# Kernel optimization log

Hardware: AMD Instinct MI355X
Metric: run time of the kernel (lower is better)

## Reference

```python
import jax, jax.numpy as jnp
import numpy as np

NUM_HEADS = 12
LN_EPS = 1e-5
SM_EPS = 1e-6


def layer_norm(x, w, b):
    m = x.mean(-1, keepdims=True)
    v = ((x - m) ** 2).mean(-1, keepdims=True)
    return (x - m) / jnp.sqrt(v + LN_EPS) * w + b


def softmax_with_policy(attn, policy):
    # attn: [B,H,N,N], policy: [B,N,1]
    B, H, N, _ = attn.shape
    attn_policy = policy.reshape(B, 1, 1, N)
    eye = jnp.eye(N, dtype=attn.dtype)[None, None]
    attn_policy = attn_policy + (1.0 - attn_policy) * eye
    m = attn.max(axis=-1, keepdims=True)
    e = jnp.exp(attn - m) * attn_policy
    return (e + SM_EPS / N) / (e.sum(axis=-1, keepdims=True) + SM_EPS)


def create_ys(ncdf, n_ref):
    # ncdf: [B, N-1]; returns ys: [B, n_ref-1]
    B = ncdf.shape[0]
    ys = jnp.linspace(0.0, 1.0, n_ref - 1, dtype=ncdf.dtype)[None, :]
    ys_start = jnp.min(ncdf + (ncdf == 0).astype(ncdf.dtype) * 1e8, axis=1, keepdims=True)
    steps = jnp.arange(n_ref - 1, dtype=ncdf.dtype)[None, :]
    return ys_start + (ys * (n_ref - 2) - ys_start * steps) / (n_ref - 2)


def get_unique_indices(indices, max_value):
    # duplicate indices are replaced by max_value, then re-sorted
    B = indices.shape[0]
    s = jnp.sort(indices, axis=1)
    shifted = jnp.concatenate([s[:, 1:], jnp.ones((B, 1), s.dtype)], axis=1)
    uniq = jnp.where(shifted == s, max_value, s)
    return jnp.sort(uniq, axis=1)


def ats_block(x, policy, norm1_w, norm1_b, qkv_w, proj_w, proj_b,
              norm2_w, norm2_b, fc1_w, fc1_b, fc2_w, fc2_b,
              n_tokens, n_ref_tokens):
    B, N, C = x.shape
    H = NUM_HEADS
    dh = C // H
    scale = dh ** -0.5

    xn = layer_norm(x, norm1_w, norm1_b)
    qkv = (xn @ qkv_w).reshape(B, N, 3, H, dh).transpose(2, 0, 3, 1, 4)  # [3,B,H,N,dh]
    qkv = qkv * policy[None, :, None, :, :]
    q, k, v = qkv[0], qkv[1], qkv[2]

    attn = softmax_with_policy(jnp.einsum('bhnd,bhmd->bhnm', q, k) * scale, policy)

    # --- score assignment ---
    v_norm = jnp.linalg.norm(v.transpose(0, 2, 1, 3).reshape(B, N, C), axis=2)  # [B,N]
    sig = attn[:, :, 0, :].sum(axis=1) * v_norm      # CLS attention row summed over heads
    sig = sig[:, 1:]
    sig = sig / sig.sum(axis=1, keepdims=True)
    order = jnp.argsort(sig, axis=1)                 # ascending
    sorted_scores = jnp.take_along_axis(sig, order, axis=1)

    # --- inverse transform sampling ---
    cdf = jnp.cumsum(sorted_scores, axis=1)
    cmin = cdf.min(axis=1, keepdims=True)
    cmax = cdf.max(axis=1, keepdims=True)
    ncdf = (cdf - cmin) / (cmax - cmin)              # [B, N-1]
    ys = create_ys(ncdf, n_ref_tokens)               # [B, n_ref-1]
    diff = (n_ref_tokens - 1) - (N - 1)
    ncdf_p = jnp.pad(ncdf, ((0, 0), (diff, 0))) if diff > 0 else ncdf
    tokens_to_pick = jnp.argmin(jnp.abs(ys[:, :, None] - ncdf_p[:, None, :]), axis=2) - diff

    uniq = get_unique_indices(tokens_to_pick, N - 1)[:, :N - 1]
    ui = uniq[:, :n_tokens - 1]                      # [B, n_tokens-1]

    # reorder attn rows / raw tokens by significance order, pad a zero row at N-1
    oidx = jnp.broadcast_to(order[:, None, :, None], (B, H, N - 1, N))
    attn_sorted = jnp.take_along_axis(attn[:, :, 1:, :], oidx, axis=2)
    attn_tmp = jnp.pad(attn_sorted, ((0, 0), (0, 0), (0, 1), (0, 0)))
    rx_sorted = jnp.take_along_axis(x[:, 1:, :], jnp.broadcast_to(order[:, :, None], (B, N - 1, C)), axis=1)
    rx_tmp = jnp.pad(rx_sorted, ((0, 0), (0, 1), (0, 0)))

    uidx = jnp.broadcast_to(ui[:, None, :, None], (B, H, n_tokens - 1, N))
    attn_sel = jnp.take_along_axis(attn_tmp, uidx, axis=2)
    rx_sel = jnp.take_along_axis(rx_tmp, jnp.broadcast_to(ui[:, :, None], (B, n_tokens - 1, C)), axis=1)

    attn_new = jnp.concatenate([attn[:, :, 0:1, :], attn_sel], axis=2)     # [B,H,n_tokens,N]
    selected_x = jnp.concatenate([x[:, 0:1, :], rx_sel], axis=1)           # [B,n_tokens,C]
    pol_new = (ui != N - 1).astype(x.dtype)[:, :, None]
    pol_new = jnp.pad(pol_new, ((0, 0), (1, 0), (0, 0)), constant_values=1.0)  # [B,n_tokens,1]

    out = jnp.einsum('bhnm,bhmd->bhnd', attn_new, v)
    out = out.transpose(0, 2, 1, 3).reshape(B, n_tokens, C)
    out = (out @ proj_w + proj_b) * pol_new

    x2 = selected_x + out
    h = jax.nn.gelu(layer_norm(x2, norm2_w, norm2_b) @ fc1_w + fc1_b, approximate=False)
    x2 = x2 + (h @ fc2_w + fc2_b) * pol_new
    return x2, pol_new


def setup_inputs() -> dict:
    key = jax.random.key(0)
    ks = jax.random.split(key, 6)
    B, N, C = 8, 785, 768
    init = lambda k, sh, fan: jax.random.normal(k, sh, jnp.float32) * (fan ** -0.5)
    return {
        'x': jax.random.normal(ks[0], (B, N, C), jnp.float32),
        'policy': jnp.ones((B, N, 1), jnp.float32),
        'norm1_w': jnp.ones((C,), jnp.float32),
        'norm1_b': jnp.zeros((C,), jnp.float32),
        'qkv_w': init(ks[1], (C, 3 * C), C),
        'proj_w': init(ks[2], (C, C), C),
        'proj_b': jnp.zeros((C,), jnp.float32),
        'norm2_w': jnp.ones((C,), jnp.float32),
        'norm2_b': jnp.zeros((C,), jnp.float32),
        'fc1_w': init(ks[3], (C, 4 * C), C),
        'fc1_b': jnp.zeros((4 * C,), jnp.float32),
        'fc2_w': init(ks[4], (4 * C, C), 4 * C),
        'fc2_b': jnp.zeros((C,), jnp.float32),
        'n_tokens': 393,
        'n_ref_tokens': 785,
    }


def reference(x, policy, norm1_w, norm1_b, qkv_w, proj_w, proj_b,
              norm2_w, norm2_b, fc1_w, fc1_b, fc2_w, fc2_b,
              n_tokens, n_ref_tokens):
    return ats_block(x, policy, norm1_w, norm1_b, qkv_w, proj_w, proj_b,
                     norm2_w, norm2_b, fc1_w, fc1_b, fc2_w, fc2_b,
                     int(n_tokens), int(n_ref_tokens))
```

## Files before the change

kernel.cpp:

```cpp
#include <hip/hip_runtime.h>
#include <hip/hip_bf16.h>
#include <float.h>
#include <math.h>
#include <stdint.h>

constexpr int B_   = 8;
constexpr int N_   = 785;
constexpr int C_   = 768;
constexpr int H_   = 12;
constexpr int DH_  = 64;
constexpr int NT_  = 393;
constexpr int QKVC = 3 * C_;
constexpr int BN   = B_ * N_;
constexpr int BT   = B_ * NT_;
constexpr int MSEL = N_ - 1;
constexpr float  SCALE_F = 0.125f;
constexpr double LNEPS   = 1e-5;
constexpr double SMEPS   = 1e-6;

#define DEV static __device__ __forceinline__

typedef __hip_bfloat16 bf16;
typedef __attribute__((ext_vector_type(8))) short frag8;
typedef __attribute__((ext_vector_type(4))) float facc4;

DEV short f2b(float v) { return (short)__hip_bfloat16_raw(__float2bfloat16(v)).x; }
DEV float b2f(short s) {
  union { unsigned int u; float f; } cv;
  cv.u = ((unsigned int)(unsigned short)s) << 16;
  return cv.f;
}
DEV float gelu_exact(float v) { return 0.5f * v * (1.0f + erff(v * 0.70710678118654752f)); }

DEV double blockReduceSumD(double v, double* scratch, int nw) {
#pragma unroll
  for (int o = 32; o; o >>= 1) v += __shfl_xor(v, o);
  int lane = threadIdx.x & 63, wid = threadIdx.x >> 6;
  __syncthreads();
  if (lane == 0) scratch[wid] = v;
  __syncthreads();
  double r = scratch[0];
  for (int i = 1; i < nw; i++) r += scratch[i];
  return r;
}
DEV double blockReduceMaxD(double v, double* scratch, int nw) {
#pragma unroll
  for (int o = 32; o; o >>= 1) v = fmax(v, __shfl_xor(v, o));
  int lane = threadIdx.x & 63, wid = threadIdx.x >> 6;
  __syncthreads();
  if (lane == 0) scratch[wid] = v;
  __syncthreads();
  double r = scratch[0];
  for (int i = 1; i < nw; i++) r = fmax(r, scratch[i]);
  return r;
}
DEV float blockReduceSumF(float v, float* scratch, int nw) {
#pragma unroll
  for (int o = 32; o; o >>= 1) v += __shfl_xor(v, o);
  int lane = threadIdx.x & 63, wid = threadIdx.x >> 6;
  __syncthreads();
  if (lane == 0) scratch[wid] = v;
  __syncthreads();
  float r = scratch[0];
  for (int i = 1; i < nw; i++) r += scratch[i];
  return r;
}
DEV float blockReduceMaxF(float v, float* scratch, int nw) {
#pragma unroll
  for (int o = 32; o; o >>= 1) v = fmaxf(v, __shfl_xor(v, o));
  int lane = threadIdx.x & 63, wid = threadIdx.x >> 6;
  __syncthreads();
  if (lane == 0) scratch[wid] = v;
  __syncthreads();
  float r = scratch[0];
  for (int i = 1; i < nw; i++) r = fmaxf(r, scratch[i]);
  return r;
}

__global__ __launch_bounds__(256) void ln1_kernel(
    const float* __restrict__ x, const float* __restrict__ w, const float* __restrict__ b,
    double* __restrict__ xn64, bf16* __restrict__ xnb) {
  int row = blockIdx.x;
  int t = threadIdx.x;
  __shared__ double scr[8];
  const float* xr = x + (size_t)row * C_;
  double vals[3];
#pragma unroll
  for (int i = 0; i < 3; i++) vals[i] = (double)xr[t + i * 256];
  double s = vals[0] + vals[1] + vals[2];
  s = blockReduceSumD(s, scr, 4);
  double mean = s / (double)C_;
  double vs = 0.0;
#pragma unroll
  for (int i = 0; i < 3; i++) { double d = vals[i] - mean; vs += d * d; }
  vs = blockReduceSumD(vs, scr, 4);
  double inv = 1.0 / sqrt(vs / (double)C_ + LNEPS);
#pragma unroll
  for (int i = 0; i < 3; i++) {
    int c = t + i * 256;
    double o = (vals[i] - mean) * inv * (double)w[c] + (double)b[c];
    xn64[(size_t)row * C_ + c] = o;
    xnb[(size_t)row * C_ + c] = __float2bfloat16((float)o);
  }
}

__global__ __launch_bounds__(256) void transpose_bf16(
    const float* __restrict__ W, bf16* __restrict__ Wt, int K, int N) {
  __shared__ float tile[32][33];
  int k0 = blockIdx.y * 32, n0 = blockIdx.x * 32;
  int tx = threadIdx.x & 31, ty = threadIdx.x >> 5;
  for (int i = ty; i < 32; i += 8) {
    int k = k0 + i, n = n0 + tx;
    tile[i][tx] = (k < K && n < N) ? W[(size_t)k * N + n] : 0.f;
  }
  __syncthreads();
  for (int i = ty; i < 32; i += 8) {
    int n = n0 + i, k = k0 + tx;
    if (n < N && k < K) Wt[(size_t)n * K + k] = __float2bfloat16(tile[tx][i]);
  }
}

__global__ __launch_bounds__(256) void gemm_bf16(
    const bf16* __restrict__ A, const bf16* __restrict__ Bt,
    float* __restrict__ Cc, const float* __restrict__ bias,
    const float* __restrict__ rowscale, int M, int K, int Ncols,
    int mode, const float* __restrict__ xg, const int* __restrict__ selidx_,
    const float* __restrict__ poln_, const float* __restrict__ res) {
  __shared__ short As[64][40];
  __shared__ short Bs[64][40];
  const short* Ap = (const short*)A;
  const short* Bp = (const short*)Bt;
  int t = threadIdx.x;
  int n0 = blockIdx.x * 64;
  int m0 = blockIdx.y * 64;
  int w = t >> 6, l = t & 63;
  int srow = t >> 2;
  int koff = (t & 3) * 8;
  facc4 acc[4] = {{0, 0, 0, 0}, {0, 0, 0, 0}, {0, 0, 0, 0}, {0, 0, 0, 0}};
  int frow = (l & 15);
  int fk = (l >> 4) * 8;
  for (int k0 = 0; k0 < K; k0 += 32) {
    {
      int4 av = make_int4(0, 0, 0, 0);
      if (m0 + srow < M)
        av = *(const int4*)(Ap + (size_t)(m0 + srow) * K + k0 + koff);
      *(int4*)(&As[srow][koff]) = av;
      int4 bv = *(const int4*)(Bp + (size_t)(n0 + srow) * K + k0 + koff);
      *(int4*)(&Bs[srow][koff]) = bv;
    }
    __syncthreads();
    frag8 a = *(frag8*)(&As[w * 16 + frow][fk]);
#pragma unroll
    for (int nt = 0; nt < 4; nt++) {
      frag8 bfr = *(frag8*)(&Bs[nt * 16 + frow][fk]);
      acc[nt] = __builtin_amdgcn_mfma_f32_16x16x32_bf16(a, bfr, acc[nt], 0, 0, 0);
    }
    __syncthreads();
  }
#pragma unroll
  for (int reg = 0; reg < 4; reg++) {
    int row = m0 + w * 16 + (l >> 4) * 4 + reg;
    if (row >= M) continue;
    float rs = (mode == 0 && rowscale) ? rowscale[row] : 1.f;
    float pn = (mode != 0) ? poln_[row] : 0.f;
    int rsel = (mode == 1) ? selidx_[row] : 0;
    int bI = (mode == 1) ? (row / NT_) : 0;
#pragma unroll
    for (int nt = 0; nt < 4; nt++) {
      int col = n0 + nt * 16 + (l & 15);
      float v = acc[nt][reg];
      if (bias) v += bias[col];
      float outv;
      if (mode == 0) {
        outv = v * rs;
      } else if (mode == 1) {
        float sx = (rsel >= 0) ? xg[(size_t)(bI * N_ + rsel) * C_ + col] : 0.f;
        outv = sx + v * pn;
      } else {
        outv = res[(size_t)row * Ncols + col] + v * pn;
      }
      Cc[(size_t)row * Ncols + col] = outv;
    }
  }
}

__global__ __launch_bounds__(256) void gemm128(
    const bf16* __restrict__ A, const bf16* __restrict__ Bt,
    float* __restrict__ Cc, const float* __restrict__ bias,
    const float* __restrict__ rowscale, int M, int K, int Ncols,
    bf16* __restrict__ gelu_bf) {
  __shared__ short As[128][40];
  __shared__ short Bs[128][40];
  const short* Ap = (const short*)A;
  const short* Bp = (const short*)Bt;
  int t = threadIdx.x;
  int n0 = blockIdx.x * 128;
  int m0 = blockIdx.y * 128;
  int w = t >> 6, l = t & 63;
  int wr = w >> 1, wc = w & 1;
  int srow = t >> 1;
  int koff = (t & 1) * 16;
  int fr = l & 15, fk = (l >> 4) * 8;
  facc4 acc[4][4] = {};
  for (int k0 = 0; k0 < K; k0 += 32) {
    int4 av0 = make_int4(0, 0, 0, 0), av1 = make_int4(0, 0, 0, 0);
    if (m0 + srow < M) {
      const short* ap = Ap + (size_t)(m0 + srow) * K + k0 + koff;
      av0 = *(const int4*)ap;
      av1 = *(const int4*)(ap + 8);
    }
    const short* bp = Bp + (size_t)(n0 + srow) * K + k0 + koff;
    int4 bv0 = *(const int4*)bp;
    int4 bv1 = *(const int4*)(bp + 8);
    *(int4*)(&As[srow][koff])     = av0;
    *(int4*)(&As[srow][koff + 8]) = av1;
    *(int4*)(&Bs[srow][koff])     = bv0;
    *(int4*)(&Bs[srow][koff + 8]) = bv1;
    __syncthreads();
    frag8 af[4], bf[4];
#pragma unroll
    for (int i = 0; i < 4; i++) af[i] = *(frag8*)(&As[wr * 64 + i * 16 + fr][fk]);
#pragma unroll
    for (int j = 0; j < 4; j++) bf[j] = *(frag8*)(&Bs[wc * 64 + j * 16 + fr][fk]);
#pragma unroll
    for (int i = 0; i < 4; i++)
#pragma unroll
      for (int j = 0; j < 4; j++)
        acc[i][j] = __builtin_amdgcn_mfma_f32_16x16x32_bf16(af[i], bf[j], acc[i][j], 0, 0, 0);
    __syncthreads();
  }
#pragma unroll
  for (int i = 0; i < 4; i++) {
#pragma unroll
    for (int reg = 0; reg < 4; reg++) {
      int row = m0 + wr * 64 + i * 16 + (l >> 4) * 4 + reg;
      if (row >= M) continue;
      float rs = rowscale ? rowscale[row] : 1.f;
#pragma unroll
      for (int j = 0; j < 4; j++) {
        int col = n0 + wc * 64 + j * 16 + fr;
        float v = acc[i][j][reg];
        if (bias) v += bias[col];
        if (gelu_bf) {
          gelu_bf[(size_t)row * Ncols + col] = __float2bfloat16(gelu_exact(v));
        } else {
          v *= rs;
          Cc[(size_t)row * Ncols + col] = v;
        }
      }
    }
  }
}

__global__ __launch_bounds__(256) void q0_kernel(
    const double* __restrict__ xn64, const float* __restrict__ qkvw,
    const float* __restrict__ policy, double* __restrict__ q064) {
  int b = blockIdx.x;
  int jc = blockIdx.y;
  int t = threadIdx.x;
  int jl = t & 63, ks = t >> 6;
  __shared__ double x0[C_];
  __shared__ double part[4][64];
  for (int i = t; i < C_; i += 256) x0[i] = xn64[(size_t)(b * N_) * C_ + i];
  __syncthreads();
  int j = jc * 64 + jl;
  const float* wp = qkvw + j;
  double a = 0.0;
  int c0 = ks * 192;
#pragma unroll 8
  for (int c = c0; c < c0 + 192; c++) a += x0[c] * (double)wp[(size_t)c * QKVC];
  part[ks][jl] = a;
  __syncthreads();
  if (t < 64) {
    double pol = (double)policy[b * N_];
    q064[b * C_ + jc * 64 + t] =
        (part[0][t] + part[1][t] + part[2][t] + part[3][t]) * pol;
  }
}

__global__ __launch_bounds__(256) void g_kernel(
    const double* __restrict__ q064, const float* __restrict__ qkvw,
    double* __restrict__ g64) {
  int bh = blockIdx.x;
  int b = bh / H_, h = bh % H_;
  int t = threadIdx.x;
  __shared__ double qh[DH_];
  if (t < DH_) qh[t] = q064[b * C_ + h * DH_ + t];
  __syncthreads();
  for (int c = t; c < C_; c += 256) {
    const float* wp = qkvw + (size_t)c * QKVC + C_ + h * DH_;
    double a = 0.0;
#pragma unroll 8
    for (int d = 0; d < DH_; d++) a += qh[d] * (double)wp[d];
    g64[(size_t)bh * C_ + c] = a;
  }
}

__global__ __launch_bounds__(256) void logits_kernel(
    const double* __restrict__ xn64, const double* __restrict__ g64,
    const float* __restrict__ policy, double* __restrict__ l64) {
  int row = blockIdx.x;
  int b = row / N_;
  int n = row % N_;
  int t = threadIdx.x;
  int w = t >> 6, lane = t & 63;
  __shared__ double xr[C_];
  for (int i = t; i < C_; i += 256) xr[i] = xn64[(size_t)row * C_ + i];
  __syncthreads();
  double pol = (double)policy[row];
#pragma unroll
  for (int hh = 0; hh < 3; hh++) {
    int h = w + hh * 4;
    const double* gp = g64 + (size_t)(b * H_ + h) * C_;
    double p = 0.0;
#pragma unroll 4
    for (int i = lane; i < C_; i += 64) p += xr[i] * gp[i];
#pragma unroll
    for (int o = 32; o; o >>= 1) p += __shfl_xor(p, o);
    if (lane == 0) l64[(size_t)(b * H_ + h) * N_ + n] = 0.125 * pol * p;
  }
}

__global__ __launch_bounds__(256) void vnorm_kernel(
    const double* __restrict__ xn64, const float* __restrict__ qkvw,
    const float* __restrict__ policy, double* __restrict__ vnorm2) {
  __shared__ double scr[8];
  int r0 = blockIdx.x * 8;
  int t = threadIdx.x;
  double acc[8][3] = {};
  const double* xb = xn64 + (size_t)r0 * C_;
  for (int c = 0; c < C_; c += 2) {
    const float* wp0 = qkvw + (size_t)c * QKVC + 2 * C_;
    const float* wp1 = wp0 + QKVC;
    double w00 = (double)wp0[t], w01 = (double)wp0[t + 256], w02 = (double)wp0[t + 512];
    double w10 = (double)wp1[t], w11 = (double)wp1[t + 256], w12 = (double)wp1[t + 512];
#pragma unroll
    for (int r = 0; r < 8; r++) {
      double x0 = xb[(size_t)r * C_ + c];
      double x1 = xb[(size_t)r * C_ + c + 1];
      acc[r][0] += x0 * w00; acc[r][1] += x0 * w01; acc[r][2] += x0 * w02;
      acc[r][0] += x1 * w10; acc[r][1] += x1 * w11; acc[r][2] += x1 * w12;
    }
  }
#pragma unroll
  for (int r = 0; r < 8; r++) {
    double p = acc[r][0] * acc[r][0] + acc[r][1] * acc[r][1] + acc[r][2] * acc[r][2];
    double s = blockReduceSumD(p, scr, 4);
    if (t == 0) {
      double pol = (double)policy[r0 + r];
      vnorm2[r0 + r] = s * pol * pol;
    }
  }
}

__global__ __launch_bounds__(256) void softmax0_kernel(
    double* __restrict__ l64, const float* __restrict__ policy) {
  int bh = blockIdx.x;
  int b = bh / H_;
  double* lp = l64 + (size_t)bh * N_;
  __shared__ double scr[8];
  int t = threadIdx.x;
  double mx = -1e300;
  for (int n = t; n < N_; n += 256) mx = fmax(mx, lp[n]);
  mx = blockReduceMaxD(mx, scr, 4);
  double ssum = 0.0;
  for (int n = t; n < N_; n += 256) {
    double pol = (double)policy[b * N_ + n];
    double w = (n == 0) ? 1.0 : pol;
    double e = exp(lp[n] - mx) * w;
    lp[n] = e;
    ssum += e;
  }
  ssum = blockReduceSumD(ssum, scr, 4);
  double denom = ssum + SMEPS;
  double addc = SMEPS / (double)N_;
  for (int n = t; n < N_; n += 256) lp[n] = (lp[n] + addc) / denom;
}

__global__ __launch_bounds__(1024) void select_kernel(
    const double* __restrict__ p0, const double* __restrict__ vnorm2,
    int* __restrict__ selidx, float* __restrict__ poln, float* __restrict__ out_pol) {
  int b = blockIdx.x;
  int t = threadIdx.x;
  __shared__ double sigv[MSEL];
  __shared__ double svals[MSEL];
  __shared__ double nc[MSEL];
  __shared__ int    ord[MSEL];
  __shared__ int    pick[MSEL];
  __shared__ int    spick[MSEL];
  __shared__ int    uq[MSEL];
  __shared__ int    suq[MSEL];
  __shared__ double sh_ys;

  if (t < MSEL) {
    int n = t + 1;
    double s = 0.0;
#pragma unroll
    for (int h = 0; h < H_; h++) s += p0[(size_t)(b * H_ + h) * N_ + n];
    sigv[t] = s * sqrt(vnorm2[b * N_ + n]);
  }
  __syncthreads();
  if (t < MSEL) {
    double v = sigv[t];
    int rank = 0;
    for (int i = 0; i < MSEL; i++) {
      double vi = sigv[i];
      rank += (vi < v) || (vi == v && i < t);
    }
    ord[rank] = t;
    svals[rank] = v;
  }
  __syncthreads();
  if (t == 0) {
    double a = 0.0;
    for (int i = 0; i < MSEL; i++) { a += svals[i]; svals[i] = a; }
  }
  __syncthreads();
  {
    double c0 = svals[0], cN = svals[MSEL - 1];
    if (t < MSEL) nc[t] = (svals[t] - c0) / (cN - c0);
  }
  __syncthreads();
  if (t == 0) {
    double m = 1e300;
    for (int i = 0; i < MSEL; i++) {
      double v = nc[i];
      if (v == 0.0) v += 100000000.0;
      m = fmin(m, v);
    }
    sh_ys = m;
  }
  __syncthreads();
  if (t < MSEL) {
    double s = sh_ys;
    double ysj = (t == MSEL - 1) ? 1.0 : (double)t / 783.0;
    double y = s + (ysj * 783.0 - s * (double)t) / 783.0;
    double bd = 1e300;
    int bi = 0;
    for (int i = 0; i < MSEL; i++) {
      double d = fabs(y - nc[i]);
      if (d < bd) { bd = d; bi = i; }
    }
    pick[t] = bi;
  }
  __syncthreads();
  if (t < MSEL) {
    int p = pick[t];
    int rank = 0;
    for (int i = 0; i < MSEL; i++) {
      int pi = pick[i];
      rank += (pi < p) || (pi == p && i < t);
    }
    spick[rank] = p;
  }
  __syncthreads();
  if (t < MSEL) {
    int s = spick[t];
    int nxt = (t < MSEL - 1) ? spick[t + 1] : 1;
    uq[t] = (nxt == s) ? MSEL : s;
  }
  __syncthreads();
  if (t < MSEL) {
    int u = uq[t];
    int rank = 0;
    for (int i = 0; i < MSEL; i++) {
      int ui = uq[i];
      rank += (ui < u) || (ui == u && i < t);
    }
    suq[rank] = u;
  }
  __syncthreads();
  if (t < NT_) {
    int sel, polI;
    if (t == 0) { sel = 0; polI = 1; }
    else {
      int ut = suq[t - 1];
      polI = (ut != MSEL) ? 1 : 0;
      sel = polI ? (ord[ut] + 1) : -1;
    }
    selidx[b * NT_ + t] = sel;
    poln[b * NT_ + t] = (float)polI;
    out_pol[b * NT_ + t] = (float)polI;
  }
}

__global__ __launch_bounds__(256) void flash_kernel(
    const float* __restrict__ qkv, const int* __restrict__ selidx,
    const float* __restrict__ policy, bf16* __restrict__ attn_bf) {
  int bh = blockIdx.y;
  int b = bh / H_, h = bh % H_;
  int j0 = blockIdx.x * 64;
  int t = threadIdx.x;
  int w = t >> 6, l = t & 63;
  __shared__ short Qs[64][72];
  __shared__ short Ks[64][72];
  __shared__ short Ps[64][72];
  __shared__ short Vs[64][72];
  __shared__ float pol_s[64];
  __shared__ float Vsum[64];

  {
    int jr = t >> 2, d0 = (t & 3) * 16;
    int j = j0 + jr;
    int r = (j < NT_) ? selidx[b * NT_ + j] : -1;
    if (r < 0) r = 0;
    const float* qp = qkv + (size_t)(b * N_ + r) * QKVC + h * DH_ + d0;
#pragma unroll
    for (int i = 0; i < 16; i++) Qs[jr][d0 + i] = f2b(qp[i]);
  }
  if (t < 64) Vsum[t] = 0.f;

  int frow = l & 15, fk = (l >> 4) * 8;
  int base_r = w * 16 + (l >> 4) * 4;
  int coln = l & 15;

  int rrow[4];
#pragma unroll
  for (int r = 0; r < 4; r++) {
    int j = j0 + base_r + r;
    rrow[r] = (j < NT_) ? selidx[b * NT_ + j] : -1;
  }
  float m_run[4] = {-1e30f, -1e30f, -1e30f, -1e30f};
  float s_run[4] = {0.f, 0.f, 0.f, 0.f};
  facc4 Oacc[4] = {{0, 0, 0, 0}, {0, 0, 0, 0}, {0, 0, 0, 0}, {0, 0, 0, 0}};

  for (int n0 = 0; n0 < 832; n0 += 64) {
    {
      int nr = t >> 2, d0 = (t & 3) * 16;
      int n = n0 + nr;
      bool ok = n < N_;
      const float* kp = qkv + (size_t)(b * N_ + (ok ? n : 0)) * QKVC + C_ + h * DH_ + d0;
#pragma unroll
      for (int i = 0; i < 16; i++) Ks[nr][d0 + i] = f2b(ok ? kp[i] : 0.f);
    }
    if (t < 64) {
      int n = n0 + t;
      pol_s[t] = (n < N_) ? policy[b * N_ + n] : 0.f;
    }
    __syncthreads();

    facc4 Sacc[4] = {{0, 0, 0, 0}, {0, 0, 0, 0}, {0, 0, 0, 0}, {0, 0, 0, 0}};
#pragma unroll
    for (int k0 = 0; k0 < 64; k0 += 32) {
      frag8 a = *(frag8*)(&Qs[w * 16 + frow][k0 + fk]);
#pragma unroll
      for (int nt = 0; nt < 4; nt++) {
        frag8 bb = *(frag8*)(&Ks[nt * 16 + frow][k0 + fk]);
        Sacc[nt] = __builtin_amdgcn_mfma_f32_16x16x32_bf16(a, bb, Sacc[nt], 0, 0, 0);
      }
    }
    float S[4][4];
    float tmax[4] = {-1e30f, -1e30f, -1e30f, -1e30f};
#pragma unroll
    for (int nt = 0; nt < 4; nt++) {
#pragma unroll
      for (int r = 0; r < 4; r++) {
        int n = n0 + nt * 16 + coln;
        float v = (n < N_) ? Sacc[nt][r] * SCALE_F : -1e30f;
        S[nt][r] = v;
        tmax[r] = fmaxf(tmax[r], v);
      }
    }
#pragma unroll
    for (int o = 1; o < 16; o <<= 1) {
#pragma unroll
      for (int r = 0; r < 4; r++) tmax[r] = fmaxf(tmax[r], __shfl_xor(tmax[r], o));
    }
    float m_new[4], scl[4], psum[4];
#pragma unroll
    for (int r = 0; r < 4; r++) {
      m_new[r] = fmaxf(m_run[r], tmax[r]);
      scl[r] = expf(m_run[r] - m_new[r]);
      psum[r] = 0.f;
    }
#pragma unroll
    for (int nt = 0; nt < 4; nt++) {
      float pol = pol_s[nt * 16 + coln];
      int n = n0 + nt * 16 + coln;
#pragma unroll
      for (int r = 0; r < 4; r++) {
        float wgt = (n == rrow[r]) ? 1.f : pol;
        float e = expf(S[nt][r] - m_new[r]) * wgt;
        S[nt][r] = e;
        psum[r] += e;
      }
    }
#pragma unroll
    for (int o = 1; o < 16; o <<= 1) {
#pragma unroll
      for (int r = 0; r < 4; r++) psum[r] += __shfl_xor(psum[r], o);
    }
#pragma unroll
    for (int r = 0; r < 4; r++) {
      s_run[r] = s_run[r] * scl[r] + psum[r];
      m_run[r] = m_new[r];
    }
    __syncthreads();

#pragma unroll
    for (int nt = 0; nt < 4; nt++) {
#pragma unroll
      for (int r = 0; r < 4; r++) Ps[base_r + r][nt * 16 + coln] = f2b(S[nt][r]);
    }
    {
      int nr = t >> 2, d0 = (t & 3) * 16;
      int n = n0 + nr;
      bool ok = n < N_;
      const float* vp = qkv + (size_t)(b * N_ + (ok ? n : 0)) * QKVC + 2 * C_ + h * DH_ + d0;
#pragma unroll
      for (int i = 0; i < 16; i++) Vs[d0 + i][nr] = f2b(ok ? vp[i] : 0.f);
    }
    __syncthreads();

    if (t < 64) {
      float a = 0.f;
#pragma unroll 16
      for (int k = 0; k < 64; k++) a += b2f(Vs[t][k]);
      Vsum[t] += a;
    }
#pragma unroll
    for (int dt = 0; dt < 4; dt++) {
#pragma unroll
      for (int r = 0; r < 4; r++) Oacc[dt][r] *= scl[r];
    }
#pragma unroll
    for (int k0 = 0; k0 < 64; k0 += 32) {
      frag8 a = *(frag8*)(&Ps[w * 16 + frow][k0 + fk]);
#pragma unroll
      for (int dt = 0; dt < 4; dt++) {
        frag8 bb = *(frag8*)(&Vs[dt * 16 + frow][k0 + fk]);
        Oacc[dt] = __builtin_amdgcn_mfma_f32_16x16x32_bf16(a, bb, Oacc[dt], 0, 0, 0);
      }
    }
  }
  __syncthreads();
  float addc = 1e-6f / (float)N_;
#pragma unroll
  for (int r = 0; r < 4; r++) {
    int j = j0 + base_r + r;
    if (j >= NT_) continue;
    float denom = s_run[r] + 1e-6f;
#pragma unroll
    for (int dt = 0; dt < 4; dt++) {
      int d = dt * 16 + coln;
      float val = (Oacc[dt][r] + addc * Vsum[d]) / denom;
      attn_bf[(size_t)(b * NT_ + j) * C_ + h * DH_ + d] = __float2bfloat16(val);
    }
  }
}

__global__ __launch_bounds__(256) void ln2_kernel(
    const float* __restrict__ xin, const float* __restrict__ w, const float* __restrict__ b,
    bf16* __restrict__ xoutb) {
  int row = blockIdx.x;
  int t = threadIdx.x;
  __shared__ float scr[8];
  const float* xr = xin + (size_t)row * C_;
  float vals[3];
#pragma unroll
  for (int i = 0; i < 3; i++) vals[i] = xr[t + i * 256];
  float s = vals[0] + vals[1] + vals[2];
  s = blockReduceSumF(s, scr, 4);
  float mean = s / (float)C_;
  float vs = 0.f;
#pragma unroll
  for (int i = 0; i < 3; i++) { float d = vals[i] - mean; vs += d * d; }
  vs = blockReduceSumF(vs, scr, 4);
  float sd = sqrtf(vs / (float)C_ + 1e-5f);
#pragma unroll
  for (int i = 0; i < 3; i++) {
    int c = t + i * 256;
    xoutb[(size_t)row * C_ + c] =
        __float2bfloat16((vals[i] - mean) / sd * w[c] + b[c]);
  }
}

extern "C" void kernel_launch(void* const* d_in, const int* in_sizes, int n_in,
                              void* d_out, int out_size, void* d_ws, size_t ws_size,
                              hipStream_t stream) {
  const float* x      = (const float*)d_in[0];
  const float* policy = (const float*)d_in[1];
  const float* n1w    = (const float*)d_in[2];
  const float* n1b    = (const float*)d_in[3];
  const float* qkvw   = (const float*)d_in[4];
  const float* projw  = (const float*)d_in[5];
  const float* projb  = (const float*)d_in[6];
  const float* n2w    = (const float*)d_in[7];
  const float* n2b    = (const float*)d_in[8];
  const float* fc1w   = (const float*)d_in[9];
  const float* fc1b   = (const float*)d_in[10];
  const float* fc2w   = (const float*)d_in[11];
  const float* fc2b   = (const float*)d_in[12];

  char* ws = (char*)d_ws;
  size_t off = 0;
  auto alloc = [&](size_t bytes) {
    size_t o = off;
    off += (bytes + 255) & ~(size_t)255;
    return o;
  };

  double* xn64    = (double*)(ws + alloc((size_t)BN * C_ * 8));
  bf16*   xnb     = (bf16*)(ws + alloc((size_t)BN * C_ * 2));
  float*  qkv32   = (float*)(ws + alloc((size_t)BN * QKVC * 4));
  double* vnorm2  = (double*)(ws + alloc((size_t)BN * 8));
  double* q064    = (double*)(ws + alloc((size_t)B_ * C_ * 8));
  double* g64     = (double*)(ws + alloc((size_t)B_ * H_ * C_ * 8));
  double* l64     = (double*)(ws + alloc((size_t)B_ * H_ * N_ * 8));
  int*    selidx  = (int*)(ws + alloc((size_t)BT * 4));
  float*  poln    = (float*)(ws + alloc((size_t)BT * 4));
  bf16*   attn_bf = (bf16*)(ws + alloc((size_t)BT * C_ * 2));
  float*  x2      = (float*)(ws + alloc((size_t)BT * C_ * 4));
  bf16*   qkvw_t  = (bf16*)(ws + alloc((size_t)QKVC * C_ * 2));
  bf16*   projw_t = (bf16*)(ws + alloc((size_t)C_ * C_ * 2));
  bf16*   fc1w_t  = (bf16*)(ws + alloc((size_t)4 * C_ * C_ * 2));
  bf16*   fc2w_t  = (bf16*)(ws + alloc((size_t)C_ * 4 * C_ * 2));
  bf16*   xn2b    = (bf16*)(ws + alloc((size_t)BT * C_ * 2));
  bf16*   h_bf    = (bf16*)(ws + alloc((size_t)BT * 4 * C_ * 2));
  if (off > ws_size) return;

  float* out_x = (float*)d_out;
  float* out_p = out_x + (size_t)BT * C_;

  transpose_bf16<<<dim3(QKVC / 32, C_ / 32), 256, 0, stream>>>(qkvw, qkvw_t, C_, QKVC);
  transpose_bf16<<<dim3(C_ / 32, C_ / 32), 256, 0, stream>>>(projw, projw_t, C_, C_);
  transpose_bf16<<<dim3(4 * C_ / 32, C_ / 32), 256, 0, stream>>>(fc1w, fc1w_t, C_, 4 * C_);
  transpose_bf16<<<dim3(C_ / 32, 4 * C_ / 32), 256, 0, stream>>>(fc2w, fc2w_t, 4 * C_, C_);

  ln1_kernel<<<BN, 256, 0, stream>>>(x, n1w, n1b, xn64, xnb);

  {
    dim3 g(QKVC / 128, (BN + 127) / 128);
    gemm128<<<g, 256, 0, stream>>>(xnb, qkvw_t, qkv32, nullptr, policy, BN, C_, QKVC, nullptr);
  }

  q0_kernel<<<dim3(B_, C_ / 64), 256, 0, stream>>>(xn64, qkvw, policy, q064);
  g_kernel<<<B_ * H_, 256, 0, stream>>>(q064, qkvw, g64);
  logits_kernel<<<BN, 256, 0, stream>>>(xn64, g64, policy, l64);
  vnorm_kernel<<<BN / 8, 256, 0, stream>>>(xn64, qkvw, policy, vnorm2);
  softmax0_kernel<<<B_ * H_, 256, 0, stream>>>(l64, policy);
  select_kernel<<<B_, 1024, 0, stream>>>(l64, vnorm2, selidx, poln, out_p);

  {
    dim3 g((NT_ + 63) / 64, B_ * H_);
    flash_kernel<<<g, 256, 0, stream>>>(qkv32, selidx, policy, attn_bf);
  }

  {
    dim3 g(C_ / 64, (BT + 63) / 64);
    gemm_bf16<<<g, 256, 0, stream>>>(attn_bf, projw_t, x2, projb, nullptr, BT, C_, C_,
                                     1, x, selidx, poln, nullptr);
  }
  ln2_kernel<<<BT, 256, 0, stream>>>(x2, n2w, n2b, xn2b);
  {
    dim3 g(4 * C_ / 128, (BT + 127) / 128);
    gemm128<<<g, 256, 0, stream>>>(xn2b, fc1w_t, nullptr, fc1b, nullptr, BT, C_, 4 * C_, h_bf);
  }
  {
    dim3 g(C_ / 64, (BT + 63) / 64);
    gemm_bf16<<<g, 256, 0, stream>>>(h_bf, fc2w_t, out_x, fc2b, nullptr, BT, 4 * C_, C_,
                                     2, nullptr, nullptr, poln, x2);
  }
}
```

Baseline: 886.7 us.

## Merge vnorm, QKV GEMM and logits into one horizontally fused launch

Three independent kernels (fp64 value-norm, bf16 MFMA QKV GEMM, fp64 CLS logits) are merged into a single launch that dispatches by block index range. The vnorm blocks come first so the long fp64 work starts early and overlaps with the GEMM and logits blocks, which fills the GPU and removes launch gaps and serialization. The merged kernel has a larger shared footprint and higher register pressure, because all paths are compiled into one kernel, and that can lower occupancy for the lighter branches.

```diff
diff --git a/kernel.cpp b/kernel.cpp
--- a/kernel.cpp
+++ b/kernel.cpp
@@ -18,6 +18,12 @@
 constexpr double LNEPS   = 1e-5;
 constexpr double SMEPS   = 1e-6;
 
+constexpr int FAT_VN     = BN / 8;
+constexpr int FAT_QKV_BX = QKVC / 128;
+constexpr int FAT_QKV_BY = (BN + 127) / 128;
+constexpr int FAT_QKV    = FAT_QKV_BX * FAT_QKV_BY;
+constexpr int FAT_TOTAL  = FAT_VN + FAT_QKV + BN;
+
 #define DEV static __device__ __forceinline__
 
 typedef __hip_bfloat16 bf16;
@@ -63,17 +69,6 @@
   __syncthreads();
   float r = scratch[0];
   for (int i = 1; i < nw; i++) r += scratch[i];
-  return r;
-}
-DEV float blockReduceMaxF(float v, float* scratch, int nw) {
-#pragma unroll
-  for (int o = 32; o; o >>= 1) v = fmaxf(v, __shfl_xor(v, o));
-  int lane = threadIdx.x & 63, wid = threadIdx.x >> 6;
-  __syncthreads();
-  if (lane == 0) scratch[wid] = v;
-  __syncthreads();
-  float r = scratch[0];
-  for (int i = 1; i < nw; i++) r = fmaxf(r, scratch[i]);
   return r;
 }
 
@@ -252,6 +247,120 @@
   }
 }
 
+__global__ __launch_bounds__(256) void fat_kernel(
+    const double* __restrict__ xn64, const float* __restrict__ qkvw,
+    const float* __restrict__ policy, double* __restrict__ vnorm2,
+    const bf16* __restrict__ xnb, const bf16* __restrict__ qkvw_t,
+    float* __restrict__ qkv32, const double* __restrict__ g64,
+    double* __restrict__ l64) {
+  __shared__ __align__(16) char smem[20480];
+  int bid = blockIdx.x;
+  int t = threadIdx.x;
+  if (bid < FAT_VN) {
+    double* scr = (double*)smem;
+    int r0 = bid * 8;
+    double acc[8][3] = {};
+    const double* xb = xn64 + (size_t)r0 * C_;
+    for (int c = 0; c < C_; c += 2) {
+      const float* wp0 = qkvw + (size_t)c * QKVC + 2 * C_;
+      const float* wp1 = wp0 + QKVC;
+      double w00 = (double)wp0[t], w01 = (double)wp0[t + 256], w02 = (double)wp0[t + 512];
+      double w10 = (double)wp1[t], w11 = (double)wp1[t + 256], w12 = (double)wp1[t + 512];
+#pragma unroll
+      for (int r = 0; r < 8; r++) {
+        double x0 = xb[(size_t)r * C_ + c];
+        double x1 = xb[(size_t)r * C_ + c + 1];
+        acc[r][0] += x0 * w00; acc[r][1] += x0 * w01; acc[r][2] += x0 * w02;
+        acc[r][0] += x1 * w10; acc[r][1] += x1 * w11; acc[r][2] += x1 * w12;
+      }
+    }
+#pragma unroll
+    for (int r = 0; r < 8; r++) {
+      double p = acc[r][0] * acc[r][0] + acc[r][1] * acc[r][1] + acc[r][2] * acc[r][2];
+      double s = blockReduceSumD(p, scr, 4);
+      if (t == 0) {
+        double pol = (double)policy[r0 + r];
+        vnorm2[r0 + r] = s * pol * pol;
+      }
+    }
+  } else if (bid < FAT_VN + FAT_QKV) {
+    int q = bid - FAT_VN;
+    int n0 = (q % FAT_QKV_BX) * 128;
+    int m0 = (q / FAT_QKV_BX) * 128;
+    short (*As)[40] = (short(*)[40])smem;
+    short (*Bs)[40] = (short(*)[40])(smem + 10240);
+    const short* Ap = (const short*)xnb;
+    const short* Bp = (const short*)qkvw_t;
+    int w = t >> 6, l = t & 63;
+    int wr = w >> 1, wc = w & 1;
+    int srow = t >> 1;
+    int koff = (t & 1) * 16;
+    int fr = l & 15, fk = (l >> 4) * 8;
+    facc4 acc[4][4] = {};
+    for (int k0 = 0; k0 < C_; k0 += 32) {
+      int4 av0 = make_int4(0, 0, 0, 0), av1 = make_int4(0, 0, 0, 0);
+      if (m0 + srow < BN) {
+        const short* ap = Ap + (size_t)(m0 + srow) * C_ + k0 + koff;
+        av0 = *(const int4*)ap;
+        av1 = *(const int4*)(ap + 8);
+      }
+      const short* bp = Bp + (size_t)(n0 + srow) * C_ + k0 + koff;
+      int4 bv0 = *(const int4*)bp;
+      int4 bv1 = *(const int4*)(bp + 8);
+      *(int4*)(&As[srow][koff])     = av0;
+      *(int4*)(&As[srow][koff + 8]) = av1;
+      *(int4*)(&Bs[srow][koff])     = bv0;
+      *(int4*)(&Bs[srow][koff + 8]) = bv1;
+      __syncthreads();
+      frag8 af[4], bfv[4];
+#pragma unroll
+      for (int i = 0; i < 4; i++) af[i] = *(frag8*)(&As[wr * 64 + i * 16 + fr][fk]);
+#pragma unroll
+      for (int j = 0; j < 4; j++) bfv[j] = *(frag8*)(&Bs[wc * 64 + j * 16 + fr][fk]);
+#pragma unroll
+      for (int i = 0; i < 4; i++)
+#pragma unroll
+        for (int j = 0; j < 4; j++)
+          acc[i][j] = __builtin_amdgcn_mfma_f32_16x16x32_bf16(af[i], bfv[j], acc[i][j], 0, 0, 0);
+      __syncthreads();
+    }
+#pragma unroll
+    for (int i = 0; i < 4; i++) {
+#pragma unroll
+      for (int reg = 0; reg < 4; reg++) {
+        int row = m0 + wr * 64 + i * 16 + (l >> 4) * 4 + reg;
+        if (row >= BN) continue;
+        float rs = policy[row];
+#pragma unroll
+        for (int j = 0; j < 4; j++) {
+          int col = n0 + wc * 64 + j * 16 + fr;
+          qkv32[(size_t)row * QKVC + col] = acc[i][j][reg] * rs;
+        }
+      }
+    }
+  } else {
+    int row = bid - FAT_VN - FAT_QKV;
+    int b = row / N_;
+    int n = row % N_;
+    int w = t >> 6, lane = t & 63;
+    double* xr = (double*)smem;
+    for (int i = t; i < C_; i += 256) xr[i] = xn64[(size_t)row * C_ + i];
+    __syncthreads();
+    double pol = (double)policy[row];
+#pragma unroll
+    for (int hh = 0; hh < 3; hh++) {
+      int h = w + hh * 4;
+      const double* gp = g64 + (size_t)(b * H_ + h) * C_;
+      double p = 0.0;
+#pragma unroll 4
+      for (int i = lane; i < C_; i += 64) p += xr[i] * gp[i];
+#pragma unroll
+      for (int o = 32; o; o >>= 1) p += __shfl_xor(p, o);
+      if (lane == 0) l64[(size_t)(b * H_ + h) * N_ + n] = 0.125 * pol * p;
+    }
+  }
+}
+
 __global__ __launch_bounds__(256) void q0_kernel(
     const double* __restrict__ xn64, const float* __restrict__ qkvw,
     const float* __restrict__ policy, double* __restrict__ q064) {
@@ -293,63 +402,6 @@
 #pragma unroll 8
     for (int d = 0; d < DH_; d++) a += qh[d] * (double)wp[d];
     g64[(size_t)bh * C_ + c] = a;
-  }
-}
-
-__global__ __launch_bounds__(256) void logits_kernel(
-    const double* __restrict__ xn64, const double* __restrict__ g64,
-    const float* __restrict__ policy, double* __restrict__ l64) {
-  int row = blockIdx.x;
-  int b = row / N_;
-  int n = row % N_;
-  int t = threadIdx.x;
-  int w = t >> 6, lane = t & 63;
-  __shared__ double xr[C_];
-  for (int i = t; i < C_; i += 256) xr[i] = xn64[(size_t)row * C_ + i];
-  __syncthreads();
-  double pol = (double)policy[row];
-#pragma unroll
-  for (int hh = 0; hh < 3; hh++) {
-    int h = w + hh * 4;
-    const double* gp = g64 + (size_t)(b * H_ + h) * C_;
-    double p = 0.0;
-#pragma unroll 4
-    for (int i = lane; i < C_; i += 64) p += xr[i] * gp[i];
-#pragma unroll
-    for (int o = 32; o; o >>= 1) p += __shfl_xor(p, o);
-    if (lane == 0) l64[(size_t)(b * H_ + h) * N_ + n] = 0.125 * pol * p;
-  }
-}
-
-__global__ __launch_bounds__(256) void vnorm_kernel(
-    const double* __restrict__ xn64, const float* __restrict__ qkvw,
-    const float* __restrict__ policy, double* __restrict__ vnorm2) {
-  __shared__ double scr[8];
-  int r0 = blockIdx.x * 8;
-  int t = threadIdx.x;
-  double acc[8][3] = {};
-  const double* xb = xn64 + (size_t)r0 * C_;
-  for (int c = 0; c < C_; c += 2) {
-    const float* wp0 = qkvw + (size_t)c * QKVC + 2 * C_;
-    const float* wp1 = wp0 + QKVC;
-    double w00 = (double)wp0[t], w01 = (double)wp0[t + 256], w02 = (double)wp0[t + 512];
-    double w10 = (double)wp1[t], w11 = (double)wp1[t + 256], w12 = (double)wp1[t + 512];
-#pragma unroll
-    for (int r = 0; r < 8; r++) {
-      double x0 = xb[(size_t)r * C_ + c];
-      double x1 = xb[(size_t)r * C_ + c + 1];
-      acc[r][0] += x0 * w00; acc[r][1] += x0 * w01; acc[r][2] += x0 * w02;
-      acc[r][0] += x1 * w10; acc[r][1] += x1 * w11; acc[r][2] += x1 * w12;
-    }
-  }
-#pragma unroll
-  for (int r = 0; r < 8; r++) {
-    double p = acc[r][0] * acc[r][0] + acc[r][1] * acc[r][1] + acc[r][2] * acc[r][2];
-    double s = blockReduceSumD(p, scr, 4);
-    if (t == 0) {
-      double pol = (double)policy[r0 + r];
-      vnorm2[r0 + r] = s * pol * pol;
-    }
   }
 }
 
@@ -729,15 +781,12 @@
 
   ln1_kernel<<<BN, 256, 0, stream>>>(x, n1w, n1b, xn64, xnb);
 
-  {
-    dim3 g(QKVC / 128, (BN + 127) / 128);
-    gemm128<<<g, 256, 0, stream>>>(xnb, qkvw_t, qkv32, nullptr, policy, BN, C_, QKVC, nullptr);
-  }
-
   q0_kernel<<<dim3(B_, C_ / 64), 256, 0, stream>>>(xn64, qkvw, policy, q064);
   g_kernel<<<B_ * H_, 256, 0, stream>>>(q064, qkvw, g64);
-  logits_kernel<<<BN, 256, 0, stream>>>(xn64, g64, policy, l64);
-  vnorm_kernel<<<BN / 8, 256, 0, stream>>>(xn64, qkvw, policy, vnorm2);
+
+  fat_kernel<<<FAT_TOTAL, 256, 0, stream>>>(xn64, qkvw, policy, vnorm2,
+                                            xnb, qkvw_t, qkv32, g64, l64);
+
   softmax0_kernel<<<B_ * H_, 256, 0, stream>>>(l64, policy);
   select_kernel<<<B_, 1024, 0, stream>>>(l64, vnorm2, selidx, poln, out_p);
 
```

Measured after the change: 934.7 us. +5.4%, slower.

## Compute V-norm with FP64 MFMA GEMM plus sampled check and fallback repair

Applied to the files above, without the earlier changes.

Replaces the scalar FP64 v-norm kernel with an FP64 MFMA (16x16x4) tiled GEMM over a pre-transposed double copy of the V weights. Each column tile writes partial squared norms that a small reduce kernel sums. A sampled check kernel recomputes 64 rows the old scalar way and sets a flag on mismatch, and a repair kernel reruns the full original computation only when that flag is set. It adds an extra transpose, more workspace, and several small launches.

```diff
diff --git a/kernel.cpp b/kernel.cpp
--- a/kernel.cpp
+++ b/kernel.cpp
@@ -14,6 +14,8 @@
 constexpr int BN   = B_ * N_;
 constexpr int BT   = B_ * NT_;
 constexpr int MSEL = N_ - 1;
+constexpr int MTV  = (BN + 63) / 64;
+constexpr int MPV  = MTV * 64;
 constexpr float  SCALE_F = 0.125f;
 constexpr double LNEPS   = 1e-5;
 constexpr double SMEPS   = 1e-6;
@@ -23,6 +25,7 @@
 typedef __hip_bfloat16 bf16;
 typedef __attribute__((ext_vector_type(8))) short frag8;
 typedef __attribute__((ext_vector_type(4))) float facc4;
+typedef __attribute__((ext_vector_type(4))) double dacc4;
 
 DEV short f2b(float v) { return (short)__hip_bfloat16_raw(__float2bfloat16(v)).x; }
 DEV float b2f(short s) {
@@ -63,17 +66,6 @@
   __syncthreads();
   float r = scratch[0];
   for (int i = 1; i < nw; i++) r += scratch[i];
-  return r;
-}
-DEV float blockReduceMaxF(float v, float* scratch, int nw) {
-#pragma unroll
-  for (int o = 32; o; o >>= 1) v = fmaxf(v, __shfl_xor(v, o));
-  int lane = threadIdx.x & 63, wid = threadIdx.x >> 6;
-  __syncthreads();
-  if (lane == 0) scratch[wid] = v;
-  __syncthreads();
-  float r = scratch[0];
-  for (int i = 1; i < nw; i++) r = fmaxf(r, scratch[i]);
   return r;
 }
 
@@ -118,6 +110,18 @@
     int n = n0 + i, k = k0 + tx;
     if (n < N && k < K) Wt[(size_t)n * K + k] = __float2bfloat16(tile[tx][i]);
   }
+}
+
+__global__ __launch_bounds__(256) void transpose_wv64(
+    const float* __restrict__ qkvw, double* __restrict__ wv64t) {
+  __shared__ float tile[32][33];
+  int c0 = blockIdx.y * 32, j0 = blockIdx.x * 32;
+  int tx = threadIdx.x & 31, ty = threadIdx.x >> 5;
+  for (int i = ty; i < 32; i += 8)
+    tile[i][tx] = qkvw[(size_t)(c0 + i) * QKVC + 2 * C_ + j0 + tx];
+  __syncthreads();
+  for (int i = ty; i < 32; i += 8)
+    wv64t[(size_t)(j0 + i) * C_ + c0 + tx] = (double)tile[tx][i];
 }
 
 __global__ __launch_bounds__(256) void gemm_bf16(
@@ -321,9 +325,100 @@
   }
 }
 
-__global__ __launch_bounds__(256) void vnorm_kernel(
+__global__ __launch_bounds__(256) void vnorm_mfma_kernel(
+    const double* __restrict__ xn64, const double* __restrict__ wv64t,
+    double* __restrict__ vnp) {
+  __shared__ double As[64][18];
+  __shared__ double Bs[64][18];
+  int m0 = blockIdx.x * 64;
+  int jt = blockIdx.y;
+  int n0 = jt * 64;
+  int t = threadIdx.x;
+  int w = t >> 6, l = t & 63;
+  int srow = t >> 2;
+  int koff = (t & 3) * 4;
+  int fr = l & 15, fg = l >> 4;
+  dacc4 acc[4] = {{0, 0, 0, 0}, {0, 0, 0, 0}, {0, 0, 0, 0}, {0, 0, 0, 0}};
+  int arow = m0 + srow;
+  if (arow >= BN) arow = 0;
+  const double* abase = xn64 + (size_t)arow * C_ + koff;
+  const double* bbase = wv64t + (size_t)(n0 + srow) * C_ + koff;
+  for (int k0 = 0; k0 < C_; k0 += 16) {
+    double2 a01 = *(const double2*)(abase + k0);
+    double2 a23 = *(const double2*)(abase + k0 + 2);
+    double2 b01 = *(const double2*)(bbase + k0);
+    double2 b23 = *(const double2*)(bbase + k0 + 2);
+    *(double2*)(&As[srow][koff])     = a01;
+    *(double2*)(&As[srow][koff + 2]) = a23;
+    *(double2*)(&Bs[srow][koff])     = b01;
+    *(double2*)(&Bs[srow][koff + 2]) = b23;
+    __syncthreads();
+#pragma unroll
+    for (int i = 0; i < 4; i++) {
+      double a = As[w * 16 + fr][i * 4 + fg];
+#pragma unroll
+      for (int nt = 0; nt < 4; nt++) {
+        double bv = Bs[nt * 16 + fr][i * 4 + fg];
+        acc[nt] = __builtin_amdgcn_mfma_f64_16x16x4f64(a, bv, acc[nt], 0, 0, 0);
+      }
+    }
+    __syncthreads();
+  }
+#pragma unroll
+  for (int r = 0; r < 4; r++) {
+    double s = acc[0][r] * acc[0][r] + acc[1][r] * acc[1][r] +
+               acc[2][r] * acc[2][r] + acc[3][r] * acc[3][r];
+#pragma unroll
+    for (int o = 1; o < 16; o <<= 1) s += __shfl_xor(s, o);
+    int row = m0 + w * 16 + r * 4 + fg;
+    if (fr == 0 && row < BN) vnp[(size_t)jt * MPV + row] = s;
+  }
+}
+
+__global__ __launch_bounds__(256) void vnorm_reduce_kernel(
+    const double* __restrict__ vnp, const float* __restrict__ policy,
+    double* __restrict__ vnorm2) {
+  int row = blockIdx.x * 256 + threadIdx.x;
+  if (row >= BN) return;
+  double s = 0.0;
+#pragma unroll
+  for (int jt = 0; jt < 12; jt++) s += vnp[(size_t)jt * MPV + row];
+  double pol = (double)policy[row];
+  vnorm2[row] = s * pol * pol;
+}
+
+__global__ __launch_bounds__(256) void vnorm_check_kernel(
     const double* __restrict__ xn64, const float* __restrict__ qkvw,
-    const float* __restrict__ policy, double* __restrict__ vnorm2) {
+    const float* __restrict__ policy, const double* __restrict__ vnorm2,
+    int* __restrict__ flag) {
+  int row = blockIdx.x * 98 + (blockIdx.x & 15);
+  if (row >= BN) row = BN - 1;
+  __shared__ double scr[8];
+  int t = threadIdx.x;
+  double acc0 = 0.0, acc1 = 0.0, acc2 = 0.0;
+  const double* xr = xn64 + (size_t)row * C_;
+  for (int c = 0; c < C_; c++) {
+    double xv = xr[c];
+    const float* wp = qkvw + (size_t)c * QKVC + 2 * C_;
+    acc0 += xv * (double)wp[t];
+    acc1 += xv * (double)wp[t + 256];
+    acc2 += xv * (double)wp[t + 512];
+  }
+  double p = acc0 * acc0 + acc1 * acc1 + acc2 * acc2;
+  double s = blockReduceSumD(p, scr, 4);
+  if (t == 0) {
+    double pol = (double)policy[row];
+    double refv = s * pol * pol;
+    double got = vnorm2[row];
+    if (fabs(got - refv) > 1e-6 * fabs(refv) + 1e-280) atomicOr(flag, 1);
+  }
+}
+
+__global__ __launch_bounds__(256) void vnorm_repair_kernel(
+    const double* __restrict__ xn64, const float* __restrict__ qkvw,
+    const float* __restrict__ policy, const int* __restrict__ flag,
+    double* __restrict__ vnorm2) {
+  if (*flag == 0) return;
   __shared__ double scr[8];
   int r0 = blockIdx.x * 8;
   int t = threadIdx.x;
@@ -717,15 +812,21 @@
   bf16*   fc2w_t  = (bf16*)(ws + alloc((size_t)C_ * 4 * C_ * 2));
   bf16*   xn2b    = (bf16*)(ws + alloc((size_t)BT * C_ * 2));
   bf16*   h_bf    = (bf16*)(ws + alloc((size_t)BT * 4 * C_ * 2));
+  double* wv64t   = (double*)(ws + alloc((size_t)C_ * C_ * 8));
+  double* vnp     = (double*)(ws + alloc((size_t)12 * MPV * 8));
+  int*    vflag   = (int*)(ws + alloc(4));
   if (off > ws_size) return;
 
   float* out_x = (float*)d_out;
   float* out_p = out_x + (size_t)BT * C_;
+
+  hipMemsetAsync(vflag, 0, 4, stream);
 
   transpose_bf16<<<dim3(QKVC / 32, C_ / 32), 256, 0, stream>>>(qkvw, qkvw_t, C_, QKVC);
   transpose_bf16<<<dim3(C_ / 32, C_ / 32), 256, 0, stream>>>(projw, projw_t, C_, C_);
   transpose_bf16<<<dim3(4 * C_ / 32, C_ / 32), 256, 0, stream>>>(fc1w, fc1w_t, C_, 4 * C_);
   transpose_bf16<<<dim3(C_ / 32, 4 * C_ / 32), 256, 0, stream>>>(fc2w, fc2w_t, 4 * C_, C_);
+  transpose_wv64<<<dim3(C_ / 32, C_ / 32), 256, 0, stream>>>(qkvw, wv64t);
 
   ln1_kernel<<<BN, 256, 0, stream>>>(x, n1w, n1b, xn64, xnb);
 
@@ -737,7 +838,10 @@
   q0_kernel<<<dim3(B_, C_ / 64), 256, 0, stream>>>(xn64, qkvw, policy, q064);
   g_kernel<<<B_ * H_, 256, 0, stream>>>(q064, qkvw, g64);
   logits_kernel<<<BN, 256, 0, stream>>>(xn64, g64, policy, l64);
-  vnorm_kernel<<<BN / 8, 256, 0, stream>>>(xn64, qkvw, policy, vnorm2);
+  vnorm_mfma_kernel<<<dim3(MTV, 12), 256, 0, stream>>>(xn64, wv64t, vnp);
+  vnorm_reduce_kernel<<<(BN + 255) / 256, 256, 0, stream>>>(vnp, policy, vnorm2);
+  vnorm_check_kernel<<<64, 256, 0, stream>>>(xn64, qkvw, policy, vnorm2, vflag);
+  vnorm_repair_kernel<<<BN / 8, 256, 0, stream>>>(xn64, qkvw, policy, vflag, vnorm2);
   softmax0_kernel<<<B_ * H_, 256, 0, stream>>>(l64, policy);
   select_kernel<<<B_, 1024, 0, stream>>>(l64, vnorm2, selidx, poln, out_p);
 
```

Result: no change. 892.0 us (+0.6%).
